# Kernel optimization log

Measured on AMD Instinct MI355X. Metric: run time of the kernel, lower is better.

The kernel has to match this reference:

```python
import jax, jax.numpy as jnp
import numpy as np


def setup_inputs() -> dict:
    key = jax.random.key(0)
    ks = jax.random.split(key, 6)
    B, S, H, O, E = 4, 2048, 4096, 4096, 4
    x = jax.random.normal(ks[0], (B, S, H), dtype=jnp.float32)
    weight = jax.random.normal(ks[1], (O, H), dtype=jnp.float32)
    bias = jax.random.normal(ks[2], (O,), dtype=jnp.float32)
    gate_w = jax.random.normal(ks[3], (E, H), dtype=jnp.float32) * 0.02
    in_channel_scale = jax.random.normal(ks[4], (E, H), dtype=jnp.float32)
    out_channel_scale = jax.random.normal(ks[5], (E, O), dtype=jnp.float32)
    return {"x": x, "weight": weight, "bias": bias, "gate_w": gate_w,
            "in_channel_scale": in_channel_scale, "out_channel_scale": out_channel_scale}


def reference(x, weight, bias, gate_w, in_channel_scale, out_channel_scale):
    *lead, H = x.shape
    O = weight.shape[0]
    xf = x.reshape(-1, H)                                   # [N, H]
    # gating: Linear(H, E, bias=False) -> softmax in fp32, cast back
    router_logits = xf @ gate_w.T                           # [N, E]
    routing_weights = jax.nn.softmax(router_logits.astype(jnp.float32), axis=1).astype(x.dtype)
    in_scale = routing_weights @ in_channel_scale           # [N, H]
    out_scale = routing_weights @ out_channel_scale         # [N, O]
    bin_w = jnp.sign(weight)                                # STE sign forward
    y = ((xf * in_scale) @ bin_w.T) * out_scale + bias      # [N, O]
    return y.reshape(*lead, O)
```

## Files before the change

### kernel.cpp

```cpp
#include <hip/hip_runtime.h>
#include <hip/hip_bf16.h>

#define H_DIM 4096
#define O_DIM 4096
#define N_ROWS 8192

typedef __bf16 bf16x8 __attribute__((ext_vector_type(8)));
typedef float  f32x4  __attribute__((ext_vector_type(4)));

__device__ __forceinline__ unsigned short f32_bf16_rne(float f) {
    unsigned int u = __builtin_bit_cast(unsigned int, f);
    u += 0x7FFFu + ((u >> 16) & 1u);
    return (unsigned short)(u >> 16);
}

__device__ __forceinline__ void gload_lds16(const unsigned short* g, unsigned short* l) {
    __builtin_amdgcn_global_load_lds((const __attribute__((address_space(1))) void*)g,
                                     (__attribute__((address_space(3))) void*)l,
                                     16, 0, 0);
}

__global__ void __launch_bounds__(256) sign_kernel(const float* __restrict__ w,
                                                   unsigned short* __restrict__ bw) {
    size_t i = ((size_t)blockIdx.x * 256 + threadIdx.x) * 4;
    float4 v = *reinterpret_cast<const float4*>(w + i);
    ushort4 o;
    o.x = v.x > 0.f ? 0x3F80 : (v.x < 0.f ? 0xBF80 : 0);
    o.y = v.y > 0.f ? 0x3F80 : (v.y < 0.f ? 0xBF80 : 0);
    o.z = v.z > 0.f ? 0x3F80 : (v.z < 0.f ? 0xBF80 : 0);
    o.w = v.w > 0.f ? 0x3F80 : (v.w < 0.f ? 0xBF80 : 0);
    *reinterpret_cast<ushort4*>(bw + i) = o;
}

__global__ void __launch_bounds__(256) route_scale_kernel(
    const float* __restrict__ x, const float* __restrict__ gate_w,
    const float* __restrict__ ics, float* __restrict__ rw_out,
    unsigned short* __restrict__ xs_out)
{
    __shared__ float red[4][4];
    const int n = blockIdx.x;
    const int t = threadIdx.x;
    const float* xr = x + (size_t)n * H_DIM;

    float4 xv[4];
    float lg[4] = {0.f, 0.f, 0.f, 0.f};
#pragma unroll
    for (int c = 0; c < 4; ++c) {
        const int idx = c * 1024 + t * 4;
        xv[c] = *reinterpret_cast<const float4*>(xr + idx);
#pragma unroll
        for (int e = 0; e < 4; ++e) {
            float4 g = *reinterpret_cast<const float4*>(gate_w + e * H_DIM + idx);
            lg[e] += xv[c].x * g.x + xv[c].y * g.y + xv[c].z * g.z + xv[c].w * g.w;
        }
    }
#pragma unroll
    for (int e = 0; e < 4; ++e) {
#pragma unroll
        for (int off = 1; off < 64; off <<= 1)
            lg[e] += __shfl_xor(lg[e], off, 64);
    }
    if ((t & 63) == 0) {
        const int w = t >> 6;
        red[w][0] = lg[0]; red[w][1] = lg[1]; red[w][2] = lg[2]; red[w][3] = lg[3];
    }
    __syncthreads();
    const float l0 = red[0][0] + red[1][0] + red[2][0] + red[3][0];
    const float l1 = red[0][1] + red[1][1] + red[2][1] + red[3][1];
    const float l2 = red[0][2] + red[1][2] + red[2][2] + red[3][2];
    const float l3 = red[0][3] + red[1][3] + red[2][3] + red[3][3];
    const float m  = fmaxf(fmaxf(l0, l1), fmaxf(l2, l3));
    const float p0 = expf(l0 - m), p1 = expf(l1 - m), p2 = expf(l2 - m), p3 = expf(l3 - m);
    const float inv = 1.f / (p0 + p1 + p2 + p3);
    const float w0 = p0 * inv, w1 = p1 * inv, w2 = p2 * inv, w3 = p3 * inv;
    if (t == 0) {
        float4 wv = make_float4(w0, w1, w2, w3);
        *reinterpret_cast<float4*>(rw_out + (size_t)n * 4) = wv;
    }
#pragma unroll
    for (int c = 0; c < 4; ++c) {
        const int idx = c * 1024 + t * 4;
        float4 i0 = *reinterpret_cast<const float4*>(ics + 0 * H_DIM + idx);
        float4 i1 = *reinterpret_cast<const float4*>(ics + 1 * H_DIM + idx);
        float4 i2 = *reinterpret_cast<const float4*>(ics + 2 * H_DIM + idx);
        float4 i3 = *reinterpret_cast<const float4*>(ics + 3 * H_DIM + idx);
        const float sx = w0 * i0.x + w1 * i1.x + w2 * i2.x + w3 * i3.x;
        const float sy = w0 * i0.y + w1 * i1.y + w2 * i2.y + w3 * i3.y;
        const float sz = w0 * i0.z + w1 * i1.z + w2 * i2.z + w3 * i3.z;
        const float sw = w0 * i0.w + w1 * i1.w + w2 * i2.w + w3 * i3.w;
        ushort4 o;
        o.x = f32_bf16_rne(xv[c].x * sx);
        o.y = f32_bf16_rne(xv[c].y * sy);
        o.z = f32_bf16_rne(xv[c].z * sz);
        o.w = f32_bf16_rne(xv[c].w * sw);
        *reinterpret_cast<ushort4*>(xs_out + (size_t)n * H_DIM + idx) = o;
    }
}


#define GATE4 asm volatile("s_waitcnt vmcnt(4)" ::: "memory")
#define GATE0 asm volatile("s_waitcnt vmcnt(0)" ::: "memory")
#define NOGATE

#define WINDOW(W, CA_, CB_, NA_, NB_, DO_STAGE, GATE_STMT, DO_READS, DO_BAR)    \
  {                                                                             \
    const int w_ = (W);                                                         \
    if (DO_STAGE) {                                                             \
      const int ks_ = w_ + 3;                                                   \
      char* sA_ = lds + (ks_ & 3) * 16384;                                      \
      char* sB_ = lds + 65536 + (ks_ & 3) * 16384;                              \
      _Pragma("unroll")                                                         \
      for (int j = 0; j < 2; ++j) {                                             \
        gload_lds16(gA + ((size_t)j * 128) * H_DIM + ks_ * 32,                  \
                    (unsigned short*)(sA_ + j * 8192 + wv * 1024));             \
        gload_lds16(gB + ((size_t)j * 128) * H_DIM + ks_ * 32,                  \
                    (unsigned short*)(sB_ + j * 8192 + wv * 1024));             \
      }                                                                         \
    }                                                                           \
    GATE_STMT;                                                                  \
    __builtin_amdgcn_sched_barrier(0);                                          \
    if (DO_READS) {                                                             \
      const int sb_ = ((w_ + 1) & 3) * 16384;                                   \
      _Pragma("unroll")                                                         \
      for (int fr = 0; fr < 8; ++fr)                                            \
        NA_[fr] = *reinterpret_cast<const bf16x8*>(lds + sb_ + aOff[fr]);       \
      _Pragma("unroll")                                                         \
      for (int ni = 0; ni < 4; ++ni)                                            \
        NB_[ni] = *reinterpret_cast<const bf16x8*>(lds + 65536 + sb_ + bOff[ni]); \
    }                                                                           \
    __builtin_amdgcn_sched_barrier(0);                                          \
    __builtin_amdgcn_s_setprio(1);                                              \
    _Pragma("unroll")                                                           \
    for (int fr = 0; fr < 8; ++fr)                                              \
      _Pragma("unroll")                                                         \
      for (int ni = 0; ni < 4; ++ni)                                            \
        acc[fr][ni] = __builtin_amdgcn_mfma_f32_16x16x32_bf16(CA_[fr], CB_[ni], \
                                                              acc[fr][ni], 0, 0, 0); \
    __builtin_amdgcn_s_setprio(0);                                              \
    __builtin_amdgcn_sched_barrier(0);                                          \
    if (DO_BAR) __builtin_amdgcn_s_barrier();                                   \
  }

__global__ void __launch_bounds__(512, 2) gemm_bin_kernel(
    const unsigned short* __restrict__ xs,
    const unsigned short* __restrict__ bw,
    const float* __restrict__ rw,
    const float* __restrict__ ocs,
    const float* __restrict__ bias,
    float* __restrict__ out)
{
    __shared__ __align__(16) char lds[131072];

    const int t  = threadIdx.x;
    const int wv = t >> 6;
    const int ln = t & 63;
    const int wr = wv >> 2;
    const int wc = wv & 3;

    const int bid = blockIdx.x;
    const int swz = (bid & 7) * 64 + (bid >> 3);
    const int rowBase = (swz >> 4) * 256;
    const int colBase = (swz & 15) * 256;

    const int s_r  = t >> 2;
    const int s_cl = (t & 3) ^ ((t >> 3) & 3);
    const unsigned short* gA = xs + (size_t)(rowBase + s_r) * H_DIM + s_cl * 8;
    const unsigned short* gB = bw + (size_t)(colBase + s_r) * H_DIM + s_cl * 8;

    int aOff[8], bOff[4];
#pragma unroll
    for (int fr = 0; fr < 8; ++fr) {
        const int row = wr * 128 + fr * 16 + (ln & 15);
        aOff[fr] = row * 64 + (((ln >> 4) ^ ((row >> 1) & 3)) << 4);
    }
#pragma unroll
    for (int ni = 0; ni < 4; ++ni) {
        const int row = wc * 64 + ni * 16 + (ln & 15);
        bOff[ni] = row * 64 + (((ln >> 4) ^ ((row >> 1) & 3)) << 4);
    }

    f32x4 acc[8][4];
#pragma unroll
    for (int i = 0; i < 8; ++i)
#pragma unroll
        for (int j = 0; j < 4; ++j) acc[i][j] = (f32x4){0.f, 0.f, 0.f, 0.f};

#pragma unroll
    for (int kt = 0; kt < 3; ++kt) {
        char* sA = lds + kt * 16384;
        char* sB = lds + 65536 + kt * 16384;
#pragma unroll
        for (int j = 0; j < 2; ++j) {
            gload_lds16(gA + ((size_t)j * 128) * H_DIM + kt * 32,
                        (unsigned short*)(sA + j * 8192 + wv * 1024));
            gload_lds16(gB + ((size_t)j * 128) * H_DIM + kt * 32,
                        (unsigned short*)(sB + j * 8192 + wv * 1024));
        }
    }
    GATE4;
    __builtin_amdgcn_s_barrier();

    bf16x8 avA[8], bvA[4], avB[8], bvB[4];
#pragma unroll
    for (int fr = 0; fr < 8; ++fr)
        avA[fr] = *reinterpret_cast<const bf16x8*>(lds + aOff[fr]);
#pragma unroll
    for (int ni = 0; ni < 4; ++ni)
        bvA[ni] = *reinterpret_cast<const bf16x8*>(lds + 65536 + bOff[ni]);

    for (int w = 0; w < 124; w += 2) {
        WINDOW(w,     avA, bvA, avB, bvB, 1, GATE4, 1, 1);
        WINDOW(w + 1, avB, bvB, avA, bvA, 1, GATE4, 1, 1);
    }
    WINDOW(124, avA, bvA, avB, bvB, 1, GATE4,  1, 1);
    WINDOW(125, avB, bvB, avA, bvA, 0, GATE0,  1, 1);
    WINDOW(126, avA, bvA, avB, bvB, 0, NOGATE, 1, 1);
    WINDOW(127, avB, bvB, avA, bvA, 0, NOGATE, 0, 0);

    float oce[4][4], bve[4];
    int cole[4];
#pragma unroll
    for (int ni = 0; ni < 4; ++ni) {
        const int col = colBase + wc * 64 + ni * 16 + (ln & 15);
        cole[ni] = col;
        oce[ni][0] = ocs[0 * O_DIM + col];
        oce[ni][1] = ocs[1 * O_DIM + col];
        oce[ni][2] = ocs[2 * O_DIM + col];
        oce[ni][3] = ocs[3 * O_DIM + col];
        bve[ni] = bias[col];
    }
#pragma unroll
    for (int fr = 0; fr < 8; ++fr) {
        float4 rwv[4];
        int rowe[4];
#pragma unroll
        for (int j = 0; j < 4; ++j) {
            const int row = rowBase + wr * 128 + fr * 16 + (ln >> 4) * 4 + j;
            rowe[j] = row;
            rwv[j] = *reinterpret_cast<const float4*>(rw + (size_t)row * 4);
        }
#pragma unroll
        for (int ni = 0; ni < 4; ++ni) {
#pragma unroll
            for (int j = 0; j < 4; ++j) {
                const float os = rwv[j].x * oce[ni][0] + rwv[j].y * oce[ni][1] +
                                 rwv[j].z * oce[ni][2] + rwv[j].w * oce[ni][3];
                out[(size_t)rowe[j] * O_DIM + cole[ni]] = acc[fr][ni][j] * os + bve[ni];
            }
        }
    }
}

extern "C" void kernel_launch(void* const* d_in, const int* in_sizes, int n_in,
                              void* d_out, int out_size, void* d_ws, size_t ws_size,
                              hipStream_t stream) {
    const float* x      = (const float*)d_in[0];
    const float* weight = (const float*)d_in[1];
    const float* bias   = (const float*)d_in[2];
    const float* gate_w = (const float*)d_in[3];
    const float* ics    = (const float*)d_in[4];
    const float* ocs    = (const float*)d_in[5];
    float* out = (float*)d_out;

    unsigned short* xs = (unsigned short*)d_ws;
    unsigned short* bw = xs + (size_t)N_ROWS * H_DIM;
    float* rw = (float*)(bw + (size_t)O_DIM * H_DIM);

    sign_kernel<<<(O_DIM * H_DIM) / (256 * 4), 256, 0, stream>>>(weight, bw);
    route_scale_kernel<<<N_ROWS, 256, 0, stream>>>(x, gate_w, ics, rw, xs);
    gemm_bin_kernel<<<(N_ROWS / 256) * (O_DIM / 256), 512, 0, stream>>>(xs, bw, rw, ocs, bias, out);
}
```

Baseline: 317.5 us.

## Shrink GEMM tile to 128x256 with 4 waves and triple-buffered LDS

The binary GEMM goes from a 256x256 tile with 8 waves and a 4-stage LDS ring to a 128x256 tile with 4 waves and a 3-stage ring (72KB LDS). Register double-buffering of fragments is dropped: each window now reads its A/B fragments from LDS right before the MFMAs, and the vmcnt gate sits after the compute. The grid doubles to 1024 blocks, and the smaller LDS footprint may let two blocks share a CU. In exchange, each block reuses its data less and LDS read latency is less hidden.

```diff
diff --git a/kernel.cpp b/kernel.cpp
--- a/kernel.cpp
+++ b/kernel.cpp
@@ -98,50 +98,44 @@
 }
 
 
-#define GATE4 asm volatile("s_waitcnt vmcnt(4)" ::: "memory")
+#define STAGE_T(SS, KT)                                                         \
+  { _Pragma("unroll")                                                           \
+    for (int j = 0; j < 2; ++j)                                                 \
+      gload_lds16(gA + ((size_t)j * 64) * H_DIM + (KT) * 32,                    \
+                  (unsigned short*)(lds + (SS) * 8192 + j * 4096 + wv * 1024)); \
+    _Pragma("unroll")                                                           \
+    for (int j = 0; j < 4; ++j)                                                 \
+      gload_lds16(gB + ((size_t)j * 64) * H_DIM + (KT) * 32,                    \
+                  (unsigned short*)(lds + 24576 + (SS) * 16384 + j * 4096 + wv * 1024)); }
+
+#define GATE6 asm volatile("s_waitcnt vmcnt(6)" ::: "memory")
 #define GATE0 asm volatile("s_waitcnt vmcnt(0)" ::: "memory")
 #define NOGATE
 
-#define WINDOW(W, CA_, CB_, NA_, NB_, DO_STAGE, GATE_STMT, DO_READS, DO_BAR)    \
+#define WIN(W, RS, SS, DO_STAGE, GATE_STMT, DO_BAR)                             \
   {                                                                             \
-    const int w_ = (W);                                                         \
-    if (DO_STAGE) {                                                             \
-      const int ks_ = w_ + 3;                                                   \
-      char* sA_ = lds + (ks_ & 3) * 16384;                                      \
-      char* sB_ = lds + 65536 + (ks_ & 3) * 16384;                              \
-      _Pragma("unroll")                                                         \
-      for (int j = 0; j < 2; ++j) {                                             \
-        gload_lds16(gA + ((size_t)j * 128) * H_DIM + ks_ * 32,                  \
-                    (unsigned short*)(sA_ + j * 8192 + wv * 1024));             \
-        gload_lds16(gB + ((size_t)j * 128) * H_DIM + ks_ * 32,                  \
-                    (unsigned short*)(sB_ + j * 8192 + wv * 1024));             \
-      }                                                                         \
-    }                                                                           \
-    GATE_STMT;                                                                  \
+    if (DO_STAGE) STAGE_T(SS, (W) + 2);                                         \
     __builtin_amdgcn_sched_barrier(0);                                          \
-    if (DO_READS) {                                                             \
-      const int sb_ = ((w_ + 1) & 3) * 16384;                                   \
-      _Pragma("unroll")                                                         \
-      for (int fr = 0; fr < 8; ++fr)                                            \
-        NA_[fr] = *reinterpret_cast<const bf16x8*>(lds + sb_ + aOff[fr]);       \
-      _Pragma("unroll")                                                         \
-      for (int ni = 0; ni < 4; ++ni)                                            \
-        NB_[ni] = *reinterpret_cast<const bf16x8*>(lds + 65536 + sb_ + bOff[ni]); \
-    }                                                                           \
-    __builtin_amdgcn_sched_barrier(0);                                          \
+    bf16x8 av[8], bv[4];                                                        \
+    _Pragma("unroll")                                                           \
+    for (int ni = 0; ni < 4; ++ni)                                              \
+      bv[ni] = *reinterpret_cast<const bf16x8*>(lds + 24576 + (RS) * 16384 + bOff[ni]); \
+    _Pragma("unroll")                                                           \
+    for (int fr = 0; fr < 8; ++fr)                                              \
+      av[fr] = *reinterpret_cast<const bf16x8*>(lds + (RS) * 8192 + aOff[fr]);  \
     __builtin_amdgcn_s_setprio(1);                                              \
     _Pragma("unroll")                                                           \
     for (int fr = 0; fr < 8; ++fr)                                              \
       _Pragma("unroll")                                                         \
       for (int ni = 0; ni < 4; ++ni)                                            \
-        acc[fr][ni] = __builtin_amdgcn_mfma_f32_16x16x32_bf16(CA_[fr], CB_[ni], \
+        acc[fr][ni] = __builtin_amdgcn_mfma_f32_16x16x32_bf16(av[fr], bv[ni],   \
                                                               acc[fr][ni], 0, 0, 0); \
     __builtin_amdgcn_s_setprio(0);                                              \
-    __builtin_amdgcn_sched_barrier(0);                                          \
+    GATE_STMT;                                                                  \
     if (DO_BAR) __builtin_amdgcn_s_barrier();                                   \
   }
 
-__global__ void __launch_bounds__(512, 2) gemm_bin_kernel(
+__global__ void __launch_bounds__(256, 2) gemm_bin_kernel(
     const unsigned short* __restrict__ xs,
     const unsigned short* __restrict__ bw,
     const float* __restrict__ rw,
@@ -149,17 +143,15 @@
     const float* __restrict__ bias,
     float* __restrict__ out)
 {
-    __shared__ __align__(16) char lds[131072];
+    __shared__ __align__(16) char lds[73728];
 
     const int t  = threadIdx.x;
     const int wv = t >> 6;
     const int ln = t & 63;
-    const int wr = wv >> 2;
-    const int wc = wv & 3;
 
     const int bid = blockIdx.x;
-    const int swz = (bid & 7) * 64 + (bid >> 3);
-    const int rowBase = (swz >> 4) * 256;
+    const int swz = (bid & 7) * 128 + (bid >> 3);
+    const int rowBase = (swz >> 4) * 128;
     const int colBase = (swz & 15) * 256;
 
     const int s_r  = t >> 2;
@@ -170,12 +162,12 @@
     int aOff[8], bOff[4];
 #pragma unroll
     for (int fr = 0; fr < 8; ++fr) {
-        const int row = wr * 128 + fr * 16 + (ln & 15);
+        const int row = fr * 16 + (ln & 15);
         aOff[fr] = row * 64 + (((ln >> 4) ^ ((row >> 1) & 3)) << 4);
     }
 #pragma unroll
     for (int ni = 0; ni < 4; ++ni) {
-        const int row = wc * 64 + ni * 16 + (ln & 15);
+        const int row = wv * 64 + ni * 16 + (ln & 15);
         bOff[ni] = row * 64 + (((ln >> 4) ^ ((row >> 1) & 3)) << 4);
     }
 
@@ -185,43 +177,24 @@
 #pragma unroll
         for (int j = 0; j < 4; ++j) acc[i][j] = (f32x4){0.f, 0.f, 0.f, 0.f};
 
-#pragma unroll
-    for (int kt = 0; kt < 3; ++kt) {
-        char* sA = lds + kt * 16384;
-        char* sB = lds + 65536 + kt * 16384;
-#pragma unroll
-        for (int j = 0; j < 2; ++j) {
-            gload_lds16(gA + ((size_t)j * 128) * H_DIM + kt * 32,
-                        (unsigned short*)(sA + j * 8192 + wv * 1024));
-            gload_lds16(gB + ((size_t)j * 128) * H_DIM + kt * 32,
-                        (unsigned short*)(sB + j * 8192 + wv * 1024));
-        }
-    }
-    GATE4;
+    STAGE_T(0, 0);
+    STAGE_T(1, 1);
+    GATE6;
     __builtin_amdgcn_s_barrier();
 
-    bf16x8 avA[8], bvA[4], avB[8], bvB[4];
-#pragma unroll
-    for (int fr = 0; fr < 8; ++fr)
-        avA[fr] = *reinterpret_cast<const bf16x8*>(lds + aOff[fr]);
-#pragma unroll
-    for (int ni = 0; ni < 4; ++ni)
-        bvA[ni] = *reinterpret_cast<const bf16x8*>(lds + 65536 + bOff[ni]);
-
-    for (int w = 0; w < 124; w += 2) {
-        WINDOW(w,     avA, bvA, avB, bvB, 1, GATE4, 1, 1);
-        WINDOW(w + 1, avB, bvB, avA, bvA, 1, GATE4, 1, 1);
-    }
-    WINDOW(124, avA, bvA, avB, bvB, 1, GATE4,  1, 1);
-    WINDOW(125, avB, bvB, avA, bvA, 0, GATE0,  1, 1);
-    WINDOW(126, avA, bvA, avB, bvB, 0, NOGATE, 1, 1);
-    WINDOW(127, avB, bvB, avA, bvA, 0, NOGATE, 0, 0);
+    for (int w = 0; w < 126; w += 3) {
+        WIN(w,     0, 2, 1, GATE6, 1);
+        WIN(w + 1, 1, 0, 1, GATE6, 1);
+        WIN(w + 2, 2, 1, 1, GATE6, 1);
+    }
+    WIN(126, 0, 0, 0, GATE0, 1);
+    WIN(127, 1, 0, 0, NOGATE, 0);
 
     float oce[4][4], bve[4];
     int cole[4];
 #pragma unroll
     for (int ni = 0; ni < 4; ++ni) {
-        const int col = colBase + wc * 64 + ni * 16 + (ln & 15);
+        const int col = colBase + wv * 64 + ni * 16 + (ln & 15);
         cole[ni] = col;
         oce[ni][0] = ocs[0 * O_DIM + col];
         oce[ni][1] = ocs[1 * O_DIM + col];
@@ -235,7 +208,7 @@
         int rowe[4];
 #pragma unroll
         for (int j = 0; j < 4; ++j) {
-            const int row = rowBase + wr * 128 + fr * 16 + (ln >> 4) * 4 + j;
+            const int row = rowBase + fr * 16 + (ln >> 4) * 4 + j;
             rowe[j] = row;
             rwv[j] = *reinterpret_cast<const float4*>(rw + (size_t)row * 4);
         }
@@ -268,5 +241,5 @@
 
     sign_kernel<<<(O_DIM * H_DIM) / (256 * 4), 256, 0, stream>>>(weight, bw);
     route_scale_kernel<<<N_ROWS, 256, 0, stream>>>(x, gate_w, ics, rw, xs);
-    gemm_bin_kernel<<<(N_ROWS / 256) * (O_DIM / 256), 512, 0, stream>>>(xs, bw, rw, ocs, bias, out);
-}
+    gemm_bin_kernel<<<(N_ROWS / 128) * (O_DIM / 256), 256, 0, stream>>>(xs, bw, rw, ocs, bias, out);
+}
```

After: 349.2 us. +10.0%, slower.

## Store binarized weights as one byte each and expand to bf16 in registers

Applied to the files above, without the earlier changes.

The sign kernel now writes one byte per weight (0x3F, 0xBF or 0) instead of a 16-bit bf16 value. The GEMM stages this byte tile into a smaller LDS buffer with a new swizzle and expands it to bf16x8 with byte-permute instructions after the MFMAs of each window. This halves B-operand global traffic, LDS footprint and LDS reads, and adds ALU permute work and one fewer outstanding load per stage (vmcnt gate changed to 3).

```diff
diff --git a/kernel.cpp b/kernel.cpp
--- a/kernel.cpp
+++ b/kernel.cpp
@@ -19,17 +19,43 @@
                                      (__attribute__((address_space(3))) void*)l,
                                      16, 0, 0);
 }
+__device__ __forceinline__ void gload_lds16b(const unsigned char* g, char* l) {
+    __builtin_amdgcn_global_load_lds((const __attribute__((address_space(1))) void*)g,
+                                     (__attribute__((address_space(3))) void*)l,
+                                     16, 0, 0);
+}
+
+__device__ __forceinline__ bf16x8 b8_to_bf16x8(uint2 raw) {
+    unsigned r0 = raw.x, r1 = raw.y;
+    unsigned s0 = (r0 & 0x01010101u) << 7;
+    unsigned s1 = (r1 & 0x01010101u) << 7;
+    uint4 o;
+    o.x = __builtin_amdgcn_perm(r0, s0, 0x05010400u);
+    o.y = __builtin_amdgcn_perm(r0, s0, 0x07030602u);
+    o.z = __builtin_amdgcn_perm(r1, s1, 0x05010400u);
+    o.w = __builtin_amdgcn_perm(r1, s1, 0x07030602u);
+    return __builtin_bit_cast(bf16x8, o);
+}
 
 __global__ void __launch_bounds__(256) sign_kernel(const float* __restrict__ w,
-                                                   unsigned short* __restrict__ bw) {
-    size_t i = ((size_t)blockIdx.x * 256 + threadIdx.x) * 4;
-    float4 v = *reinterpret_cast<const float4*>(w + i);
-    ushort4 o;
-    o.x = v.x > 0.f ? 0x3F80 : (v.x < 0.f ? 0xBF80 : 0);
-    o.y = v.y > 0.f ? 0x3F80 : (v.y < 0.f ? 0xBF80 : 0);
-    o.z = v.z > 0.f ? 0x3F80 : (v.z < 0.f ? 0xBF80 : 0);
-    o.w = v.w > 0.f ? 0x3F80 : (v.w < 0.f ? 0xBF80 : 0);
-    *reinterpret_cast<ushort4*>(bw + i) = o;
+                                                   unsigned char* __restrict__ bw) {
+    size_t i = ((size_t)blockIdx.x * 256 + threadIdx.x) * 8;
+    float4 a = *reinterpret_cast<const float4*>(w + i);
+    float4 b = *reinterpret_cast<const float4*>(w + i + 4);
+    const float* v[2] = {&a.x, &b.x};
+    unsigned int p[2];
+#pragma unroll
+    for (int d = 0; d < 2; ++d) {
+        unsigned int r = 0;
+#pragma unroll
+        for (int j = 0; j < 4; ++j) {
+            float f = v[d][j];
+            unsigned int byte = f > 0.f ? 0x3Fu : (f < 0.f ? 0xBFu : 0u);
+            r |= byte << (8 * j);
+        }
+        p[d] = r;
+    }
+    *reinterpret_cast<uint2*>(bw + i) = make_uint2(p[0], p[1]);
 }
 
 __global__ void __launch_bounds__(256) route_scale_kernel(
@@ -98,7 +124,7 @@
 }
 
 
-#define GATE4 asm volatile("s_waitcnt vmcnt(4)" ::: "memory")
+#define GATE3 asm volatile("s_waitcnt vmcnt(3)" ::: "memory")
 #define GATE0 asm volatile("s_waitcnt vmcnt(0)" ::: "memory")
 #define NOGATE
 
@@ -108,25 +134,26 @@
     if (DO_STAGE) {                                                             \
       const int ks_ = w_ + 3;                                                   \
       char* sA_ = lds + (ks_ & 3) * 16384;                                      \
-      char* sB_ = lds + 65536 + (ks_ & 3) * 16384;                              \
+      char* sB_ = lds + 65536 + (ks_ & 3) * 8192;                               \
       _Pragma("unroll")                                                         \
-      for (int j = 0; j < 2; ++j) {                                             \
+      for (int j = 0; j < 2; ++j)                                               \
         gload_lds16(gA + ((size_t)j * 128) * H_DIM + ks_ * 32,                  \
                     (unsigned short*)(sA_ + j * 8192 + wv * 1024));             \
-        gload_lds16(gB + ((size_t)j * 128) * H_DIM + ks_ * 32,                  \
-                    (unsigned short*)(sB_ + j * 8192 + wv * 1024));             \
-      }                                                                         \
+      gload_lds16b(gBb + ks_ * 32, sB_ + wv * 1024);                            \
     }                                                                           \
     GATE_STMT;                                                                  \
     __builtin_amdgcn_sched_barrier(0);                                          \
+    uint2 braw0, braw1, braw2, braw3;                                           \
     if (DO_READS) {                                                             \
-      const int sb_ = ((w_ + 1) & 3) * 16384;                                   \
+      const int sbA = ((w_ + 1) & 3) * 16384;                                   \
+      const int sbB = 65536 + ((w_ + 1) & 3) * 8192;                            \
       _Pragma("unroll")                                                         \
       for (int fr = 0; fr < 8; ++fr)                                            \
-        NA_[fr] = *reinterpret_cast<const bf16x8*>(lds + sb_ + aOff[fr]);       \
-      _Pragma("unroll")                                                         \
-      for (int ni = 0; ni < 4; ++ni)                                            \
-        NB_[ni] = *reinterpret_cast<const bf16x8*>(lds + 65536 + sb_ + bOff[ni]); \
+        NA_[fr] = *reinterpret_cast<const bf16x8*>(lds + sbA + aOff[fr]);       \
+      braw0 = *reinterpret_cast<const uint2*>(lds + sbB + bOffB[0]);            \
+      braw1 = *reinterpret_cast<const uint2*>(lds + sbB + bOffB[1]);            \
+      braw2 = *reinterpret_cast<const uint2*>(lds + sbB + bOffB[2]);            \
+      braw3 = *reinterpret_cast<const uint2*>(lds + sbB + bOffB[3]);            \
     }                                                                           \
     __builtin_amdgcn_sched_barrier(0);                                          \
     __builtin_amdgcn_s_setprio(1);                                              \
@@ -137,19 +164,25 @@
         acc[fr][ni] = __builtin_amdgcn_mfma_f32_16x16x32_bf16(CA_[fr], CB_[ni], \
                                                               acc[fr][ni], 0, 0, 0); \
     __builtin_amdgcn_s_setprio(0);                                              \
+    if (DO_READS) {                                                             \
+      NB_[0] = b8_to_bf16x8(braw0);                                             \
+      NB_[1] = b8_to_bf16x8(braw1);                                             \
+      NB_[2] = b8_to_bf16x8(braw2);                                             \
+      NB_[3] = b8_to_bf16x8(braw3);                                             \
+    }                                                                           \
     __builtin_amdgcn_sched_barrier(0);                                          \
     if (DO_BAR) __builtin_amdgcn_s_barrier();                                   \
   }
 
 __global__ void __launch_bounds__(512, 2) gemm_bin_kernel(
     const unsigned short* __restrict__ xs,
-    const unsigned short* __restrict__ bw,
+    const unsigned char*  __restrict__ bwb,
     const float* __restrict__ rw,
     const float* __restrict__ ocs,
     const float* __restrict__ bias,
     float* __restrict__ out)
 {
-    __shared__ __align__(16) char lds[131072];
+    __shared__ __align__(16) char lds[98304];
 
     const int t  = threadIdx.x;
     const int wv = t >> 6;
@@ -165,9 +198,12 @@
     const int s_r  = t >> 2;
     const int s_cl = (t & 3) ^ ((t >> 3) & 3);
     const unsigned short* gA = xs + (size_t)(rowBase + s_r) * H_DIM + s_cl * 8;
-    const unsigned short* gB = bw + (size_t)(colBase + s_r) * H_DIM + s_cl * 8;
-
-    int aOff[8], bOff[4];
+
+    const int s_colB = t >> 1;
+    const int s_mB   = (t & 1) ^ ((s_colB >> 2) & 1);
+    const unsigned char* gBb = bwb + (size_t)(colBase + s_colB) * H_DIM + s_mB * 16;
+
+    int aOff[8], bOffB[4];
 #pragma unroll
     for (int fr = 0; fr < 8; ++fr) {
         const int row = wr * 128 + fr * 16 + (ln & 15);
@@ -175,8 +211,9 @@
     }
 #pragma unroll
     for (int ni = 0; ni < 4; ++ni) {
-        const int row = wc * 64 + ni * 16 + (ln & 15);
-        bOff[ni] = row * 64 + (((ln >> 4) ^ ((row >> 1) & 3)) << 4);
+        const int col = wc * 64 + ni * 16 + (ln & 15);
+        const int kg  = ln >> 4;
+        bOffB[ni] = col * 32 + ((kg ^ ((col >> 1) & 2)) << 3);
     }
 
     f32x4 acc[8][4];
@@ -188,16 +225,14 @@
 #pragma unroll
     for (int kt = 0; kt < 3; ++kt) {
         char* sA = lds + kt * 16384;
-        char* sB = lds + 65536 + kt * 16384;
-#pragma unroll
-        for (int j = 0; j < 2; ++j) {
+        char* sB = lds + 65536 + kt * 8192;
+#pragma unroll
+        for (int j = 0; j < 2; ++j)
             gload_lds16(gA + ((size_t)j * 128) * H_DIM + kt * 32,
                         (unsigned short*)(sA + j * 8192 + wv * 1024));
-            gload_lds16(gB + ((size_t)j * 128) * H_DIM + kt * 32,
-                        (unsigned short*)(sB + j * 8192 + wv * 1024));
-        }
-    }
-    GATE4;
+        gload_lds16b(gBb + kt * 32, sB + wv * 1024);
+    }
+    GATE3;
     __builtin_amdgcn_s_barrier();
 
     bf16x8 avA[8], bvA[4], avB[8], bvB[4];
@@ -205,14 +240,16 @@
     for (int fr = 0; fr < 8; ++fr)
         avA[fr] = *reinterpret_cast<const bf16x8*>(lds + aOff[fr]);
 #pragma unroll
-    for (int ni = 0; ni < 4; ++ni)
-        bvA[ni] = *reinterpret_cast<const bf16x8*>(lds + 65536 + bOff[ni]);
+    for (int ni = 0; ni < 4; ++ni) {
+        uint2 r = *reinterpret_cast<const uint2*>(lds + 65536 + bOffB[ni]);
+        bvA[ni] = b8_to_bf16x8(r);
+    }
 
     for (int w = 0; w < 124; w += 2) {
-        WINDOW(w,     avA, bvA, avB, bvB, 1, GATE4, 1, 1);
-        WINDOW(w + 1, avB, bvB, avA, bvA, 1, GATE4, 1, 1);
-    }
-    WINDOW(124, avA, bvA, avB, bvB, 1, GATE4,  1, 1);
+        WINDOW(w,     avA, bvA, avB, bvB, 1, GATE3, 1, 1);
+        WINDOW(w + 1, avB, bvB, avA, bvA, 1, GATE3, 1, 1);
+    }
+    WINDOW(124, avA, bvA, avB, bvB, 1, GATE3,  1, 1);
     WINDOW(125, avB, bvB, avA, bvA, 0, GATE0,  1, 1);
     WINDOW(126, avA, bvA, avB, bvB, 0, NOGATE, 1, 1);
     WINDOW(127, avB, bvB, avA, bvA, 0, NOGATE, 0, 0);
@@ -263,10 +300,10 @@
     float* out = (float*)d_out;
 
     unsigned short* xs = (unsigned short*)d_ws;
-    unsigned short* bw = xs + (size_t)N_ROWS * H_DIM;
-    float* rw = (float*)(bw + (size_t)O_DIM * H_DIM);
-
-    sign_kernel<<<(O_DIM * H_DIM) / (256 * 4), 256, 0, stream>>>(weight, bw);
+    unsigned char*  bwb = (unsigned char*)(xs + (size_t)N_ROWS * H_DIM);
+    float* rw = (float*)(bwb + (size_t)O_DIM * H_DIM);
+
+    sign_kernel<<<(O_DIM * H_DIM) / (256 * 8), 256, 0, stream>>>(weight, bwb);
     route_scale_kernel<<<N_ROWS, 256, 0, stream>>>(x, gate_w, ics, rw, xs);
-    gemm_bin_kernel<<<(N_ROWS / 256) * (O_DIM / 256), 512, 0, stream>>>(xs, bw, rw, ocs, bias, out);
-}
+    gemm_bin_kernel<<<(N_ROWS / 256) * (O_DIM / 256), 512, 0, stream>>>(xs, bwb, rw, ocs, bias, out);
+}
```

Result: slower. 382.0 us (+20.3%).
